# Kernel tuning notes

Measured on AMD Instinct MI355X. Metric: run time of the kernel, lower is better.

## Reference

```python
import jax, jax.numpy as jnp
import numpy as np

N, E, D_IN, D_H = 20000, 320000, 512, 512
ALPHA = 0.1
LAMBDA = 1.0

def setup_inputs() -> dict:
    key = jax.random.key(0)
    ks = jax.random.split(key, 12)
    feat = jax.random.normal(ks[0], (N, D_IN), dtype=jnp.float32)
    src = jax.random.randint(ks[1], (E,), 0, N, dtype=jnp.int32)
    dst = jax.random.randint(ks[2], (E,), 0, N, dtype=jnp.int32)
    s = 0.05
    fc_w = jax.random.normal(ks[3], (D_H, D_IN), dtype=jnp.float32) * s  # torch Linear: [out,in]
    fc_b = jax.random.normal(ks[4], (D_H,), dtype=jnp.float32) * s
    w1_1 = jax.random.normal(ks[5], (D_H, D_H), dtype=jnp.float32) * s
    w2_1 = jax.random.normal(ks[6], (D_H, D_H), dtype=jnp.float32) * s
    b_1 = jax.random.normal(ks[7], (D_H,), dtype=jnp.float32) * s
    w1_2 = jax.random.normal(ks[8], (D_H, D_H), dtype=jnp.float32) * s
    w2_2 = jax.random.normal(ks[9], (D_H, D_H), dtype=jnp.float32) * s
    b_2 = jax.random.normal(ks[10], (D_H,), dtype=jnp.float32) * s
    return {"feat": feat, "src": src, "dst": dst, "fc_w": fc_w, "fc_b": fc_b,
            "w1_1": w1_1, "w2_1": w2_1, "b_1": b_1,
            "w1_2": w1_2, "w2_2": w2_2, "b_2": b_2}


def _gcn2_layer(h, h0, src, dst, norm, w1, w2, b, layer):
    # DGL GCN2Conv (project_initial_features=False)
    beta = float(np.log(LAMBDA / layer + 1.0))
    x = h * norm                      # [N, D]
    agg = jax.ops.segment_sum(x[src], dst, num_segments=h.shape[0])  # SpMM: sum over in-neighbors
    agg = agg * norm
    f = agg * (1.0 - ALPHA)
    f0 = h0 * ALPHA
    rst = ((1.0 - beta) * f + beta * (f @ w1)
           + (1.0 - beta) * f0 + beta * (f0 @ w2) + b)
    return jax.nn.relu(rst)


def reference(feat, src, dst, fc_w, fc_b, w1_1, w2_1, b_1, w1_2, w2_2, b_2):
    n = feat.shape[0]
    h = feat @ fc_w.T + fc_b          # initial projection
    # symmetric norm from in-degrees (clamped at 1), as in DGL
    deg = jax.ops.segment_sum(jnp.ones_like(dst, dtype=h.dtype), dst, num_segments=n)
    norm = jnp.clip(deg, 1.0, None) ** -0.5
    norm = norm[:, None]
    res = _gcn2_layer(h, h, src, dst, norm, w1_1, w2_1, b_1, layer=1)
    out = _gcn2_layer(res, h, src, dst, norm, w1_2, w2_2, b_2, layer=2)
    return out
```

## Files before the change

### kernel.cpp

```cpp
#include <hip/hip_runtime.h>
#include <hip/hip_bf16.h>
#include <stdint.h>
#include <stddef.h>

typedef __bf16 bf16_t;
typedef __bf16 bf16x4 __attribute__((ext_vector_type(4)));
typedef __bf16 bf16x8 __attribute__((ext_vector_type(8)));
typedef float floatx4 __attribute__((ext_vector_type(4)));

#define NN 20000
#define EE 320000
#define DD 512
#define CAP 96
#define BETA1 0.6931471805599453f
#define BETA2 0.40546510810816444f

__device__ __forceinline__ void gload16(const bf16_t* g, bf16_t* l) {
  __builtin_amdgcn_global_load_lds((const __attribute__((address_space(1))) uint32_t*)g,
                                   (__attribute__((address_space(3))) uint32_t*)l, 16, 0, 0);
}

__global__ void bucket_kernel(const int* __restrict__ src, const int* __restrict__ dst,
                              int* __restrict__ cnt, int* __restrict__ esrc, int E) {
  int e = blockIdx.x * 256 + threadIdx.x;
  if (e < E) {
    int d = dst[e];
    int pos = atomicAdd(&cnt[d], 1);
    if (pos < CAP) esrc[d * CAP + pos] = src[e];
  }
}

__global__ void norm_kernel(const int* __restrict__ cnt, float* __restrict__ nrm, int n) {
  int i = blockIdx.x * 256 + threadIdx.x;
  if (i < n) nrm[i] = 1.0f / sqrtf(fmaxf((float)cnt[i], 1.0f));
}

__global__ void cvt_kernel(const float* __restrict__ in, bf16_t* __restrict__ out, int n4) {
  int i = blockIdx.x * 256 + threadIdx.x;
  if (i < n4) {
    float4 v = ((const float4*)in)[i];
    bf16x4 o = {(bf16_t)v.x, (bf16_t)v.y, (bf16_t)v.z, (bf16_t)v.w};
    ((bf16x4*)out)[i] = o;
  }
}

__global__ void transpose_cat(const float* __restrict__ W1, const float* __restrict__ W2,
                              bf16_t* __restrict__ BT, int K) {
  __shared__ bf16_t tile[32][33];
  int k0 = blockIdx.y * 32;
  int n0 = blockIdx.x * 32;
  int tx = threadIdx.x, ty = threadIdx.y;
  const float* W = (k0 < 512) ? W1 : W2;
  int kk = (k0 < 512) ? k0 : (k0 - 512);
#pragma unroll
  for (int i = 0; i < 32; i += 8)
    tile[ty + i][tx] = (bf16_t)W[(size_t)(kk + ty + i) * 512 + n0 + tx];
  __syncthreads();
#pragma unroll
  for (int i = 0; i < 32; i += 8)
    BT[(size_t)(n0 + ty + i) * K + k0 + tx] = tile[tx][ty + i];
}

__global__ __launch_bounds__(256) void aggregate_kernel(
    const bf16_t* __restrict__ hin, const float* __restrict__ nrm,
    const int* __restrict__ cnt, const int* __restrict__ esrc,
    bf16_t* __restrict__ Acat) {
  int node = blockIdx.x * 4 + (threadIdx.x >> 6);
  if (node >= NN) return;
  int lane = threadIdx.x & 63;
  const int* eb = esrc + (size_t)node * CAP;
  int n_e = cnt[node];
  n_e = n_e < CAP ? n_e : CAP;

  float acc[8] = {};
  bf16x8 v0 = {}, v1 = {}, v2 = {}, v3 = {};
  float ns0 = 0, ns1 = 0, ns2 = 0, ns3 = 0;

#define LOADJ(j, idx)                                                  \
  {                                                                    \
    int s = eb[idx];                                                   \
    ns##j = nrm[s];                                                    \
    v##j = *(const bf16x8*)(hin + (size_t)s * DD + lane * 8);          \
  }

  if (0 < n_e) LOADJ(0, 0)
  if (1 < n_e) LOADJ(1, 1)
  if (2 < n_e) LOADJ(2, 2)
  if (3 < n_e) LOADJ(3, 3)

  for (int i = 0; i < n_e; i += 4) {
    {
      bf16x8 a = v0; float na = ns0;
      if (i + 4 < n_e) LOADJ(0, i + 4)
#pragma unroll
      for (int k = 0; k < 8; ++k) acc[k] += na * (float)a[k];
    }
    if (i + 1 < n_e) {
      bf16x8 a = v1; float na = ns1;
      if (i + 5 < n_e) LOADJ(1, i + 5)
#pragma unroll
      for (int k = 0; k < 8; ++k) acc[k] += na * (float)a[k];
    }
    if (i + 2 < n_e) {
      bf16x8 a = v2; float na = ns2;
      if (i + 6 < n_e) LOADJ(2, i + 6)
#pragma unroll
      for (int k = 0; k < 8; ++k) acc[k] += na * (float)a[k];
    }
    if (i + 3 < n_e) {
      bf16x8 a = v3; float na = ns3;
      if (i + 7 < n_e) LOADJ(3, i + 7)
#pragma unroll
      for (int k = 0; k < 8; ++k) acc[k] += na * (float)a[k];
    }
  }
#undef LOADJ

  float nd = 0.9f * nrm[node];
  bf16x8 ob;
#pragma unroll
  for (int k = 0; k < 8; ++k) ob[k] = (bf16_t)(nd * acc[k]);
  *(bf16x8*)(Acat + (size_t)node * 1024 + lane * 8) = ob;
}

template <int MODE>
__global__ __launch_bounds__(256) void gemm_kernel(
    const bf16_t* __restrict__ A, const bf16_t* __restrict__ BT,
    int lda, int ldb, int K, int M,
    const float* __restrict__ bias,
    const bf16_t* __restrict__ acat_ro, float beta,
    float* __restrict__ outf, bf16_t* __restrict__ outb,
    bf16_t* __restrict__ acat2) {
  __shared__ bf16_t As[2][64 * 32];
  __shared__ bf16_t Bs[2][128 * 32];

  const int bid = blockIdx.x;
  const int mt = (bid >> 5) * 8 + (bid & 7);
  const int nt = (bid >> 3) & 3;
  const int m0 = mt * 64;
  if (m0 >= M) return;
  const int n0 = nt * 128;

  const int t = threadIdx.x;
  const int lane = t & 63;
  const int w = t >> 6;
  const int wm = w & 1, wn = w >> 1;
  const int quad = lane >> 4, m16 = lane & 15;

  const int r0 = t >> 2;
  const int kc = (t & 3) ^ ((r0 >> 1) & 3);
  int arow_g = m0 + r0; arow_g = arow_g < M ? arow_g : M - 1;
  const bf16_t* agp  = A  + (size_t)arow_g * lda + kc * 8;
  const bf16_t* bgp0 = BT + (size_t)(n0 + r0) * ldb + kc * 8;
  const bf16_t* bgp1 = BT + (size_t)(n0 + 64 + r0) * ldb + kc * 8;

  floatx4 acc[2][4] = {};
  const int niter = K >> 5;

  gload16(agp,  &As[0][t * 8]);
  gload16(bgp0, &Bs[0][t * 8]);
  gload16(bgp1, &Bs[0][(t + 256) * 8]);

  for (int kt = 0; kt < niter; ++kt) {
    __syncthreads();
    const int b = kt & 1;
    if (kt + 1 < niter) {
      const int nb = b ^ 1;
      const int ko = (kt + 1) * 32;
      gload16(agp + ko,  &As[nb][t * 8]);
      gload16(bgp0 + ko, &Bs[nb][t * 8]);
      gload16(bgp1 + ko, &Bs[nb][(t + 256) * 8]);
    }

    bf16x8 af[2], bfr[4];
#pragma unroll
    for (int i = 0; i < 2; ++i) {
      int arow = wm * 32 + i * 16 + m16;
      int ac = quad ^ ((arow >> 1) & 3);
      af[i] = *(const bf16x8*)(&As[b][(arow * 4 + ac) * 8]);
    }
#pragma unroll
    for (int j = 0; j < 4; ++j) {
      int brow = wn * 64 + j * 16 + m16;
      int bc = quad ^ ((brow >> 1) & 3);
      bfr[j] = *(const bf16x8*)(&Bs[b][(brow * 4 + bc) * 8]);
    }
#pragma unroll
    for (int i = 0; i < 2; ++i)
#pragma unroll
      for (int j = 0; j < 4; ++j)
        acc[i][j] = __builtin_amdgcn_mfma_f32_16x16x32_bf16(af[i], bfr[j], acc[i][j], 0, 0, 0);
  }

#pragma unroll
  for (int i = 0; i < 2; ++i) {
#pragma unroll
    for (int j = 0; j < 4; ++j) {
      int col = n0 + wn * 64 + j * 16 + m16;
      float bv = bias[col];
#pragma unroll
      for (int p = 0; p < 4; ++p) {
        int row = m0 + wm * 32 + i * 16 + quad * 4 + p;
        if (row < M) {
          size_t idx = (size_t)row * DD + col;
          float v = acc[i][j][p];
          if constexpr (MODE == 0) {
            float hv = v + bv;
            outb[idx] = (bf16_t)hv;
            acat2[(size_t)row * 1024 + 512 + col] = (bf16_t)(0.1f * hv);
          } else {
            float fsv = (float)acat_ro[(size_t)row * 1024 + col] +
                        (float)acat_ro[(size_t)row * 1024 + 512 + col];
            float r = (1.0f - beta) * fsv + beta * v + bv;
            r = fmaxf(r, 0.0f);
            if constexpr (MODE == 1) outb[idx] = (bf16_t)r;
            else outf[idx] = r;
          }
        }
      }
    }
  }
}

extern "C" void kernel_launch(void* const* d_in, const int* in_sizes, int n_in,
                              void* d_out, int out_size, void* d_ws, size_t ws_size,
                              hipStream_t stream) {
  const float* feat = (const float*)d_in[0];
  const int* src = (const int*)d_in[1];
  const int* dst = (const int*)d_in[2];
  const float* fc_w = (const float*)d_in[3];
  const float* fc_b = (const float*)d_in[4];
  const float* w1_1 = (const float*)d_in[5];
  const float* w2_1 = (const float*)d_in[6];
  const float* b_1  = (const float*)d_in[7];
  const float* w1_2 = (const float*)d_in[8];
  const float* w2_2 = (const float*)d_in[9];
  const float* b_2  = (const float*)d_in[10];
  float* out = (float*)d_out;

  char* ws = (char*)d_ws;
  size_t off = 0;
  auto alloc = [&](size_t bytes) {
    char* p = ws + off;
    off += (bytes + 255) & ~(size_t)255;
    return p;
  };
  const size_t NDf = (size_t)NN * DD;
  bf16_t* h_bf   = (bf16_t*)alloc(NDf * sizeof(bf16_t));
  bf16_t* res_bf = (bf16_t*)alloc(NDf * sizeof(bf16_t));
  bf16_t* featb  = (bf16_t*)alloc(NDf * sizeof(bf16_t));
  bf16_t* Acat   = (bf16_t*)alloc((size_t)NN * 1024 * sizeof(bf16_t));
  bf16_t* BW0    = (bf16_t*)alloc((size_t)512 * 512 * sizeof(bf16_t));
  bf16_t* BT1    = (bf16_t*)alloc((size_t)512 * 1024 * sizeof(bf16_t));
  bf16_t* BT2    = (bf16_t*)alloc((size_t)512 * 1024 * sizeof(bf16_t));
  int*    cnt    = (int*)alloc((size_t)NN * sizeof(int));
  float*  nrm    = (float*)alloc((size_t)NN * sizeof(float));
  int*    esrc   = (int*)alloc((size_t)NN * CAP * sizeof(int));

  hipMemsetAsync(cnt, 0, (size_t)NN * sizeof(int), stream);
  bucket_kernel<<<(EE + 255) / 256, 256, 0, stream>>>(src, dst, cnt, esrc, EE);
  norm_kernel<<<(NN + 255) / 256, 256, 0, stream>>>(cnt, nrm, NN);

  cvt_kernel<<<(int)(NDf / 4 / 256), 256, 0, stream>>>(feat, featb, (int)(NDf / 4));
  cvt_kernel<<<(512 * 512 / 4) / 256, 256, 0, stream>>>(fc_w, BW0, 512 * 512 / 4);

  transpose_cat<<<dim3(16, 32), dim3(32, 8), 0, stream>>>(w1_1, w2_1, BT1, 1024);
  transpose_cat<<<dim3(16, 32), dim3(32, 8), 0, stream>>>(w1_2, w2_2, BT2, 1024);

  const int gblocks = 1280;

  gemm_kernel<0><<<gblocks, 256, 0, stream>>>(featb, BW0, 512, 512, 512, NN, fc_b,
                                              nullptr, 0.0f, nullptr, h_bf, Acat);

  aggregate_kernel<<<(NN + 3) / 4, 256, 0, stream>>>(h_bf, nrm, cnt, esrc, Acat);
  gemm_kernel<1><<<gblocks, 256, 0, stream>>>(Acat, BT1, 1024, 1024, 1024, NN, b_1,
                                              Acat, BETA1, nullptr, res_bf, nullptr);

  aggregate_kernel<<<(NN + 3) / 4, 256, 0, stream>>>(res_bf, nrm, cnt, esrc, Acat);
  gemm_kernel<2><<<gblocks, 256, 0, stream>>>(Acat, BT2, 1024, 1024, 1024, NN, b_2,
                                              Acat, BETA2, out, nullptr, nullptr);
}
```

Before: 376.9 us.

## Deepen aggregation prefetch to 8 edges and double GEMM K-tile to 64

The neighbor aggregation kernel now keeps eight edge rows in flight instead of four, to hide more gather latency per wave. The GEMM kernel loads 64-wide K tiles per stage with a new 8-chunk XOR swizzle in LDS, halving the number of barrier and prefetch iterations. The cost is more registers in the aggregation kernel and double the shared memory per GEMM block, which may lower occupancy.

```diff
diff --git a/kernel.cpp b/kernel.cpp
--- a/kernel.cpp
+++ b/kernel.cpp
@@ -73,8 +73,8 @@
   n_e = n_e < CAP ? n_e : CAP;
 
   float acc[8] = {};
-  bf16x8 v0 = {}, v1 = {}, v2 = {}, v3 = {};
-  float ns0 = 0, ns1 = 0, ns2 = 0, ns3 = 0;
+  bf16x8 v0 = {}, v1 = {}, v2 = {}, v3 = {}, v4 = {}, v5 = {}, v6 = {}, v7 = {};
+  float ns0 = 0, ns1 = 0, ns2 = 0, ns3 = 0, ns4 = 0, ns5 = 0, ns6 = 0, ns7 = 0;
 
 #define LOADJ(j, idx)                                                  \
   {                                                                    \
@@ -82,38 +82,34 @@
     ns##j = nrm[s];                                                    \
     v##j = *(const bf16x8*)(hin + (size_t)s * DD + lane * 8);          \
   }
+#define SLOT(j, i)                                                     \
+  if ((i) + (j) < n_e) {                                               \
+    bf16x8 a = v##j; float na = ns##j;                                 \
+    if ((i) + (j) + 8 < n_e) LOADJ(j, (i) + (j) + 8)                   \
+    _Pragma("unroll")                                                  \
+    for (int k = 0; k < 8; ++k) acc[k] += na * (float)a[k];            \
+  }
 
   if (0 < n_e) LOADJ(0, 0)
   if (1 < n_e) LOADJ(1, 1)
   if (2 < n_e) LOADJ(2, 2)
   if (3 < n_e) LOADJ(3, 3)
-
-  for (int i = 0; i < n_e; i += 4) {
-    {
-      bf16x8 a = v0; float na = ns0;
-      if (i + 4 < n_e) LOADJ(0, i + 4)
-#pragma unroll
-      for (int k = 0; k < 8; ++k) acc[k] += na * (float)a[k];
-    }
-    if (i + 1 < n_e) {
-      bf16x8 a = v1; float na = ns1;
-      if (i + 5 < n_e) LOADJ(1, i + 5)
-#pragma unroll
-      for (int k = 0; k < 8; ++k) acc[k] += na * (float)a[k];
-    }
-    if (i + 2 < n_e) {
-      bf16x8 a = v2; float na = ns2;
-      if (i + 6 < n_e) LOADJ(2, i + 6)
-#pragma unroll
-      for (int k = 0; k < 8; ++k) acc[k] += na * (float)a[k];
-    }
-    if (i + 3 < n_e) {
-      bf16x8 a = v3; float na = ns3;
-      if (i + 7 < n_e) LOADJ(3, i + 7)
-#pragma unroll
-      for (int k = 0; k < 8; ++k) acc[k] += na * (float)a[k];
-    }
-  }
+  if (4 < n_e) LOADJ(4, 4)
+  if (5 < n_e) LOADJ(5, 5)
+  if (6 < n_e) LOADJ(6, 6)
+  if (7 < n_e) LOADJ(7, 7)
+
+  for (int i = 0; i < n_e; i += 8) {
+    SLOT(0, i)
+    SLOT(1, i)
+    SLOT(2, i)
+    SLOT(3, i)
+    SLOT(4, i)
+    SLOT(5, i)
+    SLOT(6, i)
+    SLOT(7, i)
+  }
+#undef SLOT
 #undef LOADJ
 
   float nd = 0.9f * nrm[node];
@@ -131,8 +127,8 @@
     const bf16_t* __restrict__ acat_ro, float beta,
     float* __restrict__ outf, bf16_t* __restrict__ outb,
     bf16_t* __restrict__ acat2) {
-  __shared__ bf16_t As[2][64 * 32];
-  __shared__ bf16_t Bs[2][128 * 32];
+  __shared__ bf16_t As[2][64 * 64];
+  __shared__ bf16_t Bs[2][128 * 64];
 
   const int bid = blockIdx.x;
   const int mt = (bid >> 5) * 8 + (bid & 7);
@@ -147,50 +143,61 @@
   const int wm = w & 1, wn = w >> 1;
   const int quad = lane >> 4, m16 = lane & 15;
 
-  const int r0 = t >> 2;
-  const int kc = (t & 3) ^ ((r0 >> 1) & 3);
-  int arow_g = m0 + r0; arow_g = arow_g < M ? arow_g : M - 1;
-  const bf16_t* agp  = A  + (size_t)arow_g * lda + kc * 8;
-  const bf16_t* bgp0 = BT + (size_t)(n0 + r0) * ldb + kc * 8;
-  const bf16_t* bgp1 = BT + (size_t)(n0 + 64 + r0) * ldb + kc * 8;
+  const int tr = t >> 3;
+  const int gc = (t & 7) ^ (tr & 7);
+  int arow0 = m0 + tr;      arow0 = arow0 < M ? arow0 : M - 1;
+  int arow1 = m0 + tr + 32; arow1 = arow1 < M ? arow1 : M - 1;
+  const bf16_t* agp0 = A + (size_t)arow0 * lda + gc * 8;
+  const bf16_t* agp1 = A + (size_t)arow1 * lda + gc * 8;
+  const bf16_t* bgp0 = BT + (size_t)(n0 + tr) * ldb + gc * 8;
+  const bf16_t* bgp1 = BT + (size_t)(n0 + tr + 32) * ldb + gc * 8;
+  const bf16_t* bgp2 = BT + (size_t)(n0 + tr + 64) * ldb + gc * 8;
+  const bf16_t* bgp3 = BT + (size_t)(n0 + tr + 96) * ldb + gc * 8;
+
+#define STAGE(buf, ko)                              \
+  gload16(agp0 + (ko), &As[buf][t * 8]);            \
+  gload16(agp1 + (ko), &As[buf][(t + 256) * 8]);    \
+  gload16(bgp0 + (ko), &Bs[buf][t * 8]);            \
+  gload16(bgp1 + (ko), &Bs[buf][(t + 256) * 8]);    \
+  gload16(bgp2 + (ko), &Bs[buf][(t + 512) * 8]);    \
+  gload16(bgp3 + (ko), &Bs[buf][(t + 768) * 8]);
 
   floatx4 acc[2][4] = {};
-  const int niter = K >> 5;
-
-  gload16(agp,  &As[0][t * 8]);
-  gload16(bgp0, &Bs[0][t * 8]);
-  gload16(bgp1, &Bs[0][(t + 256) * 8]);
+  const int niter = K >> 6;
+
+  STAGE(0, 0)
 
   for (int kt = 0; kt < niter; ++kt) {
     __syncthreads();
     const int b = kt & 1;
     if (kt + 1 < niter) {
-      const int nb = b ^ 1;
-      const int ko = (kt + 1) * 32;
-      gload16(agp + ko,  &As[nb][t * 8]);
-      gload16(bgp0 + ko, &Bs[nb][t * 8]);
-      gload16(bgp1 + ko, &Bs[nb][(t + 256) * 8]);
+      const int ko = (kt + 1) * 64;
+      STAGE(b ^ 1, ko)
     }
 
-    bf16x8 af[2], bfr[4];
-#pragma unroll
-    for (int i = 0; i < 2; ++i) {
-      int arow = wm * 32 + i * 16 + m16;
-      int ac = quad ^ ((arow >> 1) & 3);
-      af[i] = *(const bf16x8*)(&As[b][(arow * 4 + ac) * 8]);
+#pragma unroll
+    for (int ks = 0; ks < 2; ++ks) {
+      bf16x8 af[2], bfr[4];
+#pragma unroll
+      for (int i = 0; i < 2; ++i) {
+        int arow = wm * 32 + i * 16 + m16;
+        int cc = (ks * 4 + quad) ^ (arow & 7);
+        af[i] = *(const bf16x8*)(&As[b][(arow * 8 + cc) * 8]);
+      }
+#pragma unroll
+      for (int j = 0; j < 4; ++j) {
+        int brow = wn * 64 + j * 16 + m16;
+        int cc = (ks * 4 + quad) ^ (brow & 7);
+        bfr[j] = *(const bf16x8*)(&Bs[b][(brow * 8 + cc) * 8]);
+      }
+#pragma unroll
+      for (int i = 0; i < 2; ++i)
+#pragma unroll
+        for (int j = 0; j < 4; ++j)
+          acc[i][j] = __builtin_amdgcn_mfma_f32_16x16x32_bf16(af[i], bfr[j], acc[i][j], 0, 0, 0);
     }
-#pragma unroll
-    for (int j = 0; j < 4; ++j) {
-      int brow = wn * 64 + j * 16 + m16;
-      int bc = quad ^ ((brow >> 1) & 3);
-      bfr[j] = *(const bf16x8*)(&Bs[b][(brow * 4 + bc) * 8]);
-    }
-#pragma unroll
-    for (int i = 0; i < 2; ++i)
-#pragma unroll
-      for (int j = 0; j < 4; ++j)
-        acc[i][j] = __builtin_amdgcn_mfma_f32_16x16x32_bf16(af[i], bfr[j], acc[i][j], 0, 0, 0);
-  }
+  }
+#undef STAGE
 
 #pragma unroll
   for (int i = 0; i < 2; ++i) {
```

New measurement: 363.1 us. 1.04x faster.
